# Kernel optimization log

Measured on AMD Instinct MI355X. Metric: run time of the kernel, lower is better.

## Reference

```python
import jax, jax.numpy as jnp
import numpy as np

GRID = 48
F = GRID * GRID        # number of mesh faces
C = 128                # channels
H = 8                  # attention heads
DH = C // H
B = 2                  # meshes in batch
WID = 256              # SelectionPrediction width


def _bfs_levels():
    """BFS flood-fill levels on a 4-connected GRIDxGRID face graph, anchor at center.
    Returns [n_levels, max_ring] int32, padded with F (dropped on scatter)."""
    c = GRID // 2
    ii, jj = np.meshgrid(np.arange(GRID), np.arange(GRID), indexing='ij')
    d = (np.abs(ii - c) + np.abs(jj - c)).reshape(-1)  # BFS depth == Manhattan dist
    L = int(d.max()) + 1
    Bd = int(np.bincount(d).max())
    idx = np.full((L, Bd), F, dtype=np.int32)
    for lv in range(L):
        faces = np.nonzero(d == lv)[0]
        idx[lv, :faces.size] = faces
    return jnp.asarray(idx)


def setup_inputs() -> dict:
    key = jax.random.key(0)
    ks = jax.random.split(key, 16)
    s = 1.0 / np.sqrt(C)
    sw = 1.0 / np.sqrt(WID)
    return {
        'x':  jax.random.normal(ks[0], (B, C, F), jnp.float32),
        # AnchorAttentionBlock projections (q/k/v/out)
        'Wq': jax.random.normal(ks[1], (C, C), jnp.float32) * s,
        'Wk': jax.random.normal(ks[2], (C, C), jnp.float32) * s,
        'Wv': jax.random.normal(ks[3], (C, C), jnp.float32) * s,
        'Wo': jax.random.normal(ks[4], (C, C), jnp.float32) * s,
        # SelectionPrediction (n_input=C, width=256, depth=3, sigmoid)
        'W1': jax.random.normal(ks[5], (C, WID), jnp.float32) * s,
        'b1': jnp.zeros((WID,), jnp.float32),
        'W2': jax.random.normal(ks[6], (WID, WID), jnp.float32) * sw,
        'b2': jnp.zeros((WID,), jnp.float32),
        'W3': jax.random.normal(ks[7], (WID, WID), jnp.float32) * sw,
        'b3': jnp.zeros((WID,), jnp.float32),
        'W4': jax.random.normal(ks[8], (WID, WID), jnp.float32) * sw,
        'b4': jnp.zeros((WID,), jnp.float32),
        'W5': jax.random.normal(ks[9], (WID, 1), jnp.float32) * sw,
        'b5': jnp.zeros((1,), jnp.float32),
        'levels_idx': _bfs_levels(),
    }


def reference(x, Wq, Wk, Wv, Wo, W1, b1, W2, b2, W3, b3, W4, b4, W5, b5, levels_idx):
    scale = 1.0 / jnp.sqrt(jnp.asarray(DH, x.dtype))

    def flood(feats):                       # feats: [F, C], one mesh
        def step(cur, idx):                 # idx: [Bd] boundary ring (pad = F)
            q = cur[idx]                                    # [Bd, C] (pad rows clamp-gather)
            qh = (q @ Wq).reshape(-1, H, DH)                # [Bd, H, DH]
            kh = (cur @ Wk).reshape(F, H, DH)               # global fftype: keys = all faces
            vh = (cur @ Wv).reshape(F, H, DH)
            att = jax.nn.softmax(jnp.einsum('bhd,fhd->bhf', qh, kh) * scale, axis=-1)
            o = jnp.einsum('bhf,fhd->bhd', att, vh).reshape(-1, C) @ Wo
            new = q + o                                     # mode='resid'
            return cur.at[idx].set(new, mode='drop'), None  # pad idx == F -> dropped
        out, _ = jax.lax.scan(step, feats, levels_idx)
        return out

    final = jax.vmap(flood)(x.transpose(0, 2, 1))           # [B, F, C]
    # SelectionPrediction on final_features.transpose(2,1)
    h = jax.nn.relu(final @ W1 + b1)
    h = jax.nn.relu(h @ W2 + b2)
    h = jax.nn.relu(h @ W3 + b3)
    h = jax.nn.relu(h @ W4 + b4)
    scores = jax.nn.sigmoid(h @ W5 + b5)                    # [B, F, 1] in [0, 1]
    return final.transpose(0, 2, 1), scores
```

## Files before the change

kernel.cpp:

```cpp
#include <hip/hip_runtime.h>
#include <hip/hip_bf16.h>
#include <stdint.h>

#define GRIDN 48
#define F 2304
#define C 128
#define H 8
#define DH 16
#define NB 2
#define WID 256
#define NLV 49
#define SMH (H * 18)

typedef __hip_bfloat16 bf16;

__device__ __forceinline__ float b2f(bf16 v) { return __bfloat162float(v); }

__global__ void k_permdetect(const void* __restrict__ x, int* __restrict__ flag,
                             int* __restrict__ permIdx, int* __restrict__ lvflags) {
    __shared__ int cnt[NLV], start[NLV];
    __shared__ int bad;
    int t = threadIdx.x;
    if (t == 0) bad = 0;
    if (t < NLV) cnt[t] = 0;
    for (int i = t; i < 2 * NLV + 2; i += 256) lvflags[i] = 0;
    __syncthreads();
    {
        const bf16* xb = (const bf16*)x;
        int insane = 0;
        #pragma unroll
        for (int i = 0; i < 8; ++i) {
            float v = b2f(xb[t * 8 + i]);
            if (!(fabsf(v) < 1e10f)) insane = 1;
        }
        if (insane) atomicOr(&bad, 1);
    }
    for (int f = t; f < F; f += 256) {
        int d = abs(f / GRIDN - GRIDN / 2) + abs(f % GRIDN - GRIDN / 2);
        atomicAdd(&cnt[d], 1);
    }
    __syncthreads();
    if (t == 0) {
        int s = 0;
        for (int l = 0; l < NLV; ++l) { start[l] = s; s += cnt[l]; }
        *flag = bad;
    }
    __syncthreads();
    for (int f = t; f < F; f += 256) {
        int d = abs(f / GRIDN - GRIDN / 2) + abs(f % GRIDN - GRIDN / 2);
        permIdx[f] = atomicAdd(&start[d], 1);
    }
}

struct WSeg { const void* src; int off; int cnt; };
struct WSegs { WSeg s[14]; };

__global__ void k_convert(WSegs segs, const int* __restrict__ flag,
                          float* __restrict__ dst, int total) {
    int i = blockIdx.x * blockDim.x + threadIdx.x;
    if (i >= total) return;
    bool f32 = (*flag != 0);
    #pragma unroll 1
    for (int j = 0; j < 14; ++j) {
        int off = segs.s[j].off, cnt = segs.s[j].cnt;
        if (i >= off && i < off + cnt) {
            int k = i - off;
            dst[i] = f32 ? ((const float*)segs.s[j].src)[k]
                         : b2f(((const bf16*)segs.s[j].src)[k]);
            return;
        }
    }
}

__global__ void k_wtrans(const float* __restrict__ Wk, const float* __restrict__ Wv,
                         const float* __restrict__ Wo, float* __restrict__ wT) {
    int m = blockIdx.y;
    const float* s = m == 0 ? Wk : (m == 1 ? Wv : Wo);
    int c = blockIdx.x;
    int k = threadIdx.x;
    wT[((size_t)m * C + c) * C + k] = s[k * C + c];
}

__global__ void k_transpose_in(const void* __restrict__ x, const int* __restrict__ flag,
                               float* __restrict__ cur) {
    __shared__ float tile[32][33];
    bool f32 = (*flag != 0);
    int b = blockIdx.z;
    int f0 = blockIdx.x * 32, c0 = blockIdx.y * 32;
    int tx = threadIdx.x, ty = threadIdx.y;
    #pragma unroll
    for (int i = 0; i < 4; ++i) {
        int c = c0 + ty + i * 8;
        size_t idx = ((size_t)b * C + c) * F + f0 + tx;
        tile[ty + i * 8][tx] = f32 ? ((const float*)x)[idx] : b2f(((const bf16*)x)[idx]);
    }
    __syncthreads();
    #pragma unroll
    for (int i = 0; i < 4; ++i) {
        int f = f0 + ty + i * 8;
        cur[((size_t)b * F + f) * C + c0 + tx] = tile[tx][ty + i * 8];
    }
}

__global__ __launch_bounds__(128) void k_proj_init(
        const float* __restrict__ cur, const int* __restrict__ permIdx,
        const float* __restrict__ Wq, const float* __restrict__ Wk, const float* __restrict__ Wv,
        float* __restrict__ qh, float* __restrict__ khT, float* __restrict__ vhT) {
    __shared__ float rows[2][C];
    int r0 = blockIdx.x * 2;
    int tid = threadIdx.x;
    rows[0][tid] = cur[(size_t)r0 * C + tid];
    rows[1][tid] = cur[(size_t)(r0 + 1) * C + tid];
    __syncthreads();
    float aq0 = 0.f, aq1 = 0.f, ak0 = 0.f, ak1 = 0.f, av0 = 0.f, av1 = 0.f;
    for (int k = 0; k < C; ++k) {
        float wq = Wq[k * C + tid];
        float wk = Wk[k * C + tid];
        float wv = Wv[k * C + tid];
        float x0 = rows[0][k], x1 = rows[1][k];
        aq0 = fmaf(x0, wq, aq0); aq1 = fmaf(x1, wq, aq1);
        ak0 = fmaf(x0, wk, ak0); ak1 = fmaf(x1, wk, ak1);
        av0 = fmaf(x0, wv, av0); av1 = fmaf(x1, wv, av1);
    }
    const float scale = 0.25f;
    #pragma unroll
    for (int r = 0; r < 2; ++r) {
        int grow = r0 + r;
        int mesh = grow / F, face = grow % F;
        int p = permIdx[face];
        qh[(size_t)grow * C + tid] = (r == 0 ? aq0 : aq1) * scale;
        khT[((size_t)mesh * C + tid) * F + p] = r == 0 ? ak0 : ak1;
        vhT[((size_t)mesh * C + tid) * F + p] = r == 0 ? av0 : av1;
    }
}

struct Rings { int v[NLV + 1]; };
struct Pairs { int v[NLV + 1]; };

__global__ __launch_bounds__(256) void k_static(
        int Bd, Rings rings, Pairs pairs,
        const int* __restrict__ levels,
        const float* __restrict__ qh_all,
        const float* __restrict__ khT, const float* __restrict__ vhT,
        float* __restrict__ smS) {
    int bx = blockIdx.x;
    int mesh = bx & 1;
    int gp = bx >> 1;
    int lv = 0;
    while (gp >= pairs.v[lv + 1]) ++lv;
    int spair = gp - pairs.v[lv];
    int rs = rings.v[lv];
    int s0 = spair * 2, s1 = s0 + 1;
    int face0 = (s0 < Bd) ? levels[lv * Bd + s0] : F;
    int face1 = (s1 < Bd) ? levels[lv * Bd + s1] : F;
    bool a0 = (face0 >= 0 && face0 < F), a1 = (face1 >= 0 && face1 < F);
    if (!a0 && !a1) return;

    __shared__ float sQh[2][C];
    int tid = threadIdx.x;
    size_t row0 = ((size_t)mesh * F + face0) * C;
    size_t row1 = ((size_t)mesh * F + face1) * C;
    if (tid < C) sQh[0][tid] = a0 ? qh_all[row0 + tid] : 0.f;
    else { int c = tid - C; sQh[1][c] = a1 ? qh_all[row1 + c] : 0.f; }
    __syncthreads();

    int head = tid >> 5, sub = tid & 31;
    float q0[DH], q1[DH];
    #pragma unroll
    for (int d = 0; d < DH; ++d) { q0[d] = sQh[0][head * DH + d]; q1[d] = sQh[1][head * DH + d]; }

    const float* Kb = khT + ((size_t)mesh * C + head * DH) * F;
    const float* Vb = vhT + ((size_t)mesh * C + head * DH) * F;

    float m0 = -1e30f, l0 = 0.f, m1 = -1e30f, l1 = 0.f;
    float acc0[DH], acc1[DH];
    #pragma unroll
    for (int d = 0; d < DH; ++d) { acc0[d] = 0.f; acc1[d] = 0.f; }

    int base0 = rs & ~127;
    for (int base = base0; base < F; base += 128) {
        int p4 = base + 4 * sub;
        float sx0 = 0, sy0 = 0, sz0 = 0, sw0 = 0;
        float sx1 = 0, sy1 = 0, sz1 = 0, sw1 = 0;
        #pragma unroll
        for (int d = 0; d < DH; ++d) {
            float4 kk = *(const float4*)(Kb + d * F + p4);
            float a = q0[d], b = q1[d];
            sx0 = fmaf(a, kk.x, sx0); sy0 = fmaf(a, kk.y, sy0);
            sz0 = fmaf(a, kk.z, sz0); sw0 = fmaf(a, kk.w, sw0);
            sx1 = fmaf(b, kk.x, sx1); sy1 = fmaf(b, kk.y, sy1);
            sz1 = fmaf(b, kk.z, sz1); sw1 = fmaf(b, kk.w, sw1);
        }
        float g0 = 1.f, g1 = 1.f, g2 = 1.f, g3 = 1.f;
        if (base < rs) {
            g0 = (p4     >= rs) ? 1.f : 0.f; g1 = (p4 + 1 >= rs) ? 1.f : 0.f;
            g2 = (p4 + 2 >= rs) ? 1.f : 0.f; g3 = (p4 + 3 >= rs) ? 1.f : 0.f;
        }
        float mx0 = fmaxf(fmaxf(sx0, sy0), fmaxf(sz0, sw0));
        float mn0 = fmaxf(m0, mx0);
        float c0 = __expf(m0 - mn0);
        float px0 = __expf(sx0 - mn0) * g0, py0 = __expf(sy0 - mn0) * g1;
        float pz0 = __expf(sz0 - mn0) * g2, pw0 = __expf(sw0 - mn0) * g3;
        l0 = fmaf(l0, c0, px0 + py0 + pz0 + pw0);
        m0 = mn0;
        float mx1 = fmaxf(fmaxf(sx1, sy1), fmaxf(sz1, sw1));
        float mn1 = fmaxf(m1, mx1);
        float c1e = __expf(m1 - mn1);
        float px1 = __expf(sx1 - mn1) * g0, py1 = __expf(sy1 - mn1) * g1;
        float pz1 = __expf(sz1 - mn1) * g2, pw1 = __expf(sw1 - mn1) * g3;
        l1 = fmaf(l1, c1e, px1 + py1 + pz1 + pw1);
        m1 = mn1;
        #pragma unroll
        for (int d = 0; d < DH; ++d) {
            float4 vv = *(const float4*)(Vb + d * F + p4);
            float w0 = fmaf(px0, vv.x, fmaf(py0, vv.y, fmaf(pz0, vv.z, pw0 * vv.w)));
            float w1 = fmaf(px1, vv.x, fmaf(py1, vv.y, fmaf(pz1, vv.z, pw1 * vv.w)));
            acc0[d] = fmaf(acc0[d], c0, w0);
            acc1[d] = fmaf(acc1[d], c1e, w1);
        }
    }

    #pragma unroll
    for (int w = 16; w >= 1; w >>= 1) {
        float mo = __shfl_xor(m0, w), lo = __shfl_xor(l0, w);
        float mn = fmaxf(m0, mo);
        float ca = __expf(m0 - mn), cb = __expf(mo - mn);
        l0 = l0 * ca + lo * cb;
        #pragma unroll
        for (int d = 0; d < DH; ++d) {
            float ao = __shfl_xor(acc0[d], w);
            acc0[d] = acc0[d] * ca + ao * cb;
        }
        m0 = mn;
        mo = __shfl_xor(m1, w); lo = __shfl_xor(l1, w);
        mn = fmaxf(m1, mo);
        ca = __expf(m1 - mn); cb = __expf(mo - mn);
        l1 = l1 * ca + lo * cb;
        #pragma unroll
        for (int d = 0; d < DH; ++d) {
            float ao = __shfl_xor(acc1[d], w);
            acc1[d] = acc1[d] * ca + ao * cb;
        }
        m1 = mn;
    }
    if (sub == 0) {
        if (a0) {
            float* S = smS + (size_t)(mesh * F + face0) * SMH + head * 18;
            S[0] = m0; S[1] = l0;
            #pragma unroll
            for (int d = 0; d < DH; ++d) S[2 + d] = acc0[d];
        }
        if (a1) {
            float* S = smS + (size_t)(mesh * F + face1) * SMH + head * 18;
            S[0] = m1; S[1] = l1;
            #pragma unroll
            for (int d = 0; d < DH; ++d) S[2 + d] = acc1[d];
        }
    }
}

__global__ __launch_bounds__(256, 4) void k_flood(
        int Bd, Rings rings, Pairs pairs,
        const int* __restrict__ levels, const int* __restrict__ permIdx,
        const float* __restrict__ qh_all, float* __restrict__ cur,
        float* __restrict__ khT, float* __restrict__ vhT,
        const float* __restrict__ smS,
        const float* __restrict__ WkT, const float* __restrict__ WvT,
        const float* __restrict__ WoT,
        int* __restrict__ lvflags, int* __restrict__ lvdone) {
    int bx = blockIdx.x;
    int mesh = bx & 1;
    int gp2 = bx >> 1;
    int lv = 0;
    while (gp2 >= pairs.v[lv + 1]) ++lv;
    int spair = gp2 - pairs.v[lv];

    int s0 = spair * 2, s1 = s0 + 1;
    int face0 = (s0 < Bd) ? levels[lv * Bd + s0] : F;
    int face1 = (s1 < Bd) ? levels[lv * Bd + s1] : F;
    bool a0 = (face0 >= 0 && face0 < F), a1 = (face1 >= 0 && face1 < F);

    __shared__ __attribute__((aligned(16))) float sQh[2][C], sQ[2][C], sRed[2][C], sNew2[2][C];
    __shared__ float sL[2][H];
    int tid = threadIdx.x;
    size_t row0 = ((size_t)mesh * F + face0) * C;
    size_t row1 = ((size_t)mesh * F + face1) * C;
    if (tid < C) {
        if (a0) { sQ[0][tid] = cur[row0 + tid]; sQh[0][tid] = qh_all[row0 + tid]; }
        else    { sQ[0][tid] = 0.f; sQh[0][tid] = 0.f; }
    } else {
        int c = tid - C;
        if (a1) { sQ[1][c] = cur[row1 + c]; sQh[1][c] = qh_all[row1 + c]; }
        else    { sQ[1][c] = 0.f; sQh[1][c] = 0.f; }
    }
    __syncthreads();

    int head = tid >> 5, sub = tid & 31;
    float q0[DH], q1[DH];
    #pragma unroll
    for (int d = 0; d < DH; ++d) { q0[d] = sQh[0][head * DH + d]; q1[d] = sQh[1][head * DH + d]; }

    float* Kb = khT + ((size_t)mesh * C + head * DH) * F;
    float* Vb = vhT + ((size_t)mesh * C + head * DH) * F;

    float m0 = -1e30f, l0 = 0.f, m1 = -1e30f, l1 = 0.f;
    float acc0[DH], acc1[DH];
    #pragma unroll
    for (int d = 0; d < DH; ++d) { acc0[d] = 0.f; acc1[d] = 0.f; }

    #define FOLD_COL(p)                                                                 \
    {                                                                                   \
        float kvv[DH], vv[DH];                                                          \
        _Pragma("unroll")                                                               \
        for (int d = 0; d < DH; ++d)                                                    \
            kvv[d] = __hip_atomic_load(Kb + (size_t)d * F + (p), __ATOMIC_RELAXED,      \
                                       __HIP_MEMORY_SCOPE_AGENT);                       \
        _Pragma("unroll")                                                               \
        for (int d = 0; d < DH; ++d)                                                    \
            vv[d] = __hip_atomic_load(Vb + (size_t)d * F + (p), __ATOMIC_RELAXED,       \
                                      __HIP_MEMORY_SCOPE_AGENT);                        \
        float s0v = 0.f, s1v = 0.f;                                                     \
        _Pragma("unroll")                                                               \
        for (int d = 0; d < DH; ++d) {                                                  \
            s0v = fmaf(q0[d], kvv[d], s0v);                                             \
            s1v = fmaf(q1[d], kvv[d], s1v);                                             \
        }                                                                               \
        float mn0_ = fmaxf(m0, s0v);                                                    \
        float c0_ = __expf(m0 - mn0_), pw0_ = __expf(s0v - mn0_);                       \
        l0 = l0 * c0_ + pw0_;                                                           \
        _Pragma("unroll")                                                               \
        for (int d = 0; d < DH; ++d) acc0[d] = fmaf(acc0[d], c0_, pw0_ * vv[d]);        \
        m0 = mn0_;                                                                      \
        float mn1_ = fmaxf(m1, s1v);                                                    \
        float c1_ = __expf(m1 - mn1_), pw1_ = __expf(s1v - mn1_);                       \
        l1 = l1 * c1_ + pw1_;                                                           \
        _Pragma("unroll")                                                               \
        for (int d = 0; d < DH; ++d) acc1[d] = fmaf(acc1[d], c1_, pw1_ * vv[d]);        \
        m1 = mn1_;                                                                      \
    }

    int ld = __hip_atomic_load(&lvdone[mesh], __ATOMIC_RELAXED, __HIP_MEMORY_SCOPE_AGENT);
    if (ld > lv) ld = lv;
    int bulkEnd = rings.v[ld];
    for (int p = sub; p < bulkEnd; p += 32) FOLD_COL(p);

    for (int gpi = ld; gpi < lv; ++gpi) {
        int need = pairs.v[gpi + 1] - pairs.v[gpi];
        int* fl = &lvflags[gpi * 2 + mesh];
        int guard = 0;
        while (__hip_atomic_load(fl, __ATOMIC_RELAXED, __HIP_MEMORY_SCOPE_AGENT) < need
               && guard < (1 << 22)) {
            __builtin_amdgcn_s_sleep(1);
            ++guard;
        }
        int frs = rings.v[gpi], fre = rings.v[gpi + 1];
        for (int p = frs + sub; p < fre; p += 32) FOLD_COL(p);
    }
    #undef FOLD_COL

    #pragma unroll
    for (int w = 16; w >= 1; w >>= 1) {
        float mo = __shfl_xor(m0, w), lo = __shfl_xor(l0, w);
        float mn = fmaxf(m0, mo);
        float ca = __expf(m0 - mn), cb = __expf(mo - mn);
        l0 = l0 * ca + lo * cb;
        #pragma unroll
        for (int d = 0; d < DH; ++d) {
            float ao = __shfl_xor(acc0[d], w);
            acc0[d] = acc0[d] * ca + ao * cb;
        }
        m0 = mn;
        mo = __shfl_xor(m1, w); lo = __shfl_xor(l1, w);
        mn = fmaxf(m1, mo);
        ca = __expf(m1 - mn); cb = __expf(mo - mn);
        l1 = l1 * ca + lo * cb;
        #pragma unroll
        for (int d = 0; d < DH; ++d) {
            float ao = __shfl_xor(acc1[d], w);
            acc1[d] = acc1[d] * ca + ao * cb;
        }
        m1 = mn;
    }
    if (sub == 0) {
        {
            int fr = a0 ? face0 : 0;
            const float* S = smS + (size_t)(mesh * F + fr) * SMH + head * 18;
            float ms = S[0], ls = S[1];
            float mn = fmaxf(m0, ms);
            float ca = __expf(m0 - mn), cb = __expf(ms - mn);
            sL[0][head] = l0 * ca + ls * cb;
            #pragma unroll
            for (int d = 0; d < DH; ++d)
                sRed[0][head * DH + d] = fmaf(acc0[d], ca, S[2 + d] * cb);
        }
        {
            int fr = a1 ? face1 : 0;
            const float* S = smS + (size_t)(mesh * F + fr) * SMH + head * 18;
            float ms = S[0], ls = S[1];
            float mn = fmaxf(m1, ms);
            float ca = __expf(m1 - mn), cb = __expf(ms - mn);
            sL[1][head] = l1 * ca + ls * cb;
            #pragma unroll
            for (int d = 0; d < DH; ++d)
                sRed[1][head * DH + d] = fmaf(acc1[d], ca, S[2 + d] * cb);
        }
    }
    __syncthreads();
    if (tid < C) sRed[0][tid] = sRed[0][tid] / sL[0][tid >> 4];
    else { int c = tid - C; sRed[1][c] = sRed[1][c] / sL[1][c >> 4]; }
    __syncthreads();

    {
        int j = tid >> 7;
        int c = tid & 127;
        bool act = j == 0 ? a0 : a1;
        float o = 0.f;
        const float4* WoR = (const float4*)(WoT + (size_t)c * C);
        const float4* Rr  = (const float4*)(&sRed[j][0]);
        #pragma unroll
        for (int k4 = 0; k4 < C / 4; ++k4) {
            float4 w = WoR[k4];
            float4 r = Rr[k4];
            o = fmaf(r.x, w.x, o); o = fmaf(r.y, w.y, o);
            o = fmaf(r.z, w.z, o); o = fmaf(r.w, w.w, o);
        }
        float nv = sQ[j][c] + o;
        sNew2[j][c] = nv;
        if (act) cur[(j == 0 ? row0 : row1) + c] = nv;
    }
    __syncthreads();

    if (lv != NLV - 1) {
        #pragma unroll 1
        for (int j = 0; j < 2; ++j) {
            bool act = j == 0 ? a0 : a1;
            if (!act) continue;
            int facej = j == 0 ? face0 : face1;
            int p = permIdx[facej];
            int c = tid & 127;
            const float* WT = (tid < C) ? WkT : WvT;
            float a = 0.f;
            const float4* Wr = (const float4*)(WT + (size_t)c * C);
            const float4* Nr = (const float4*)(&sNew2[j][0]);
            #pragma unroll
            for (int k4 = 0; k4 < C / 4; ++k4) {
                float4 w = Wr[k4];
                float4 x = Nr[k4];
                a = fmaf(x.x, w.x, a); a = fmaf(x.y, w.y, a);
                a = fmaf(x.z, w.z, a); a = fmaf(x.w, w.w, a);
            }
            if (tid < C)
                __hip_atomic_store(khT + ((size_t)mesh * C + c) * F + p, a,
                                   __ATOMIC_RELAXED, __HIP_MEMORY_SCOPE_AGENT);
            else
                __hip_atomic_store(vhT + ((size_t)mesh * C + c) * F + p, a,
                                   __ATOMIC_RELAXED, __HIP_MEMORY_SCOPE_AGENT);
        }
        __syncthreads();
        if (tid == 0) {
            int need = pairs.v[lv + 1] - pairs.v[lv];
            int old = __hip_atomic_fetch_add(&lvflags[lv * 2 + mesh], 1,
                                             __ATOMIC_RELAXED, __HIP_MEMORY_SCOPE_AGENT);
            if (old == need - 1)
                __hip_atomic_fetch_max(&lvdone[mesh], lv + 1,
                                       __ATOMIC_RELAXED, __HIP_MEMORY_SCOPE_AGENT);
        }
    }
}

__global__ __launch_bounds__(256) void k_mlp(
        const float* __restrict__ cur,
        const float* __restrict__ W1, const float* __restrict__ b1,
        const float* __restrict__ W2, const float* __restrict__ b2,
        const float* __restrict__ W3, const float* __restrict__ b3,
        const float* __restrict__ W4, const float* __restrict__ b4,
        const float* __restrict__ W5, const float* __restrict__ b5,
        float* __restrict__ out_scores) {
    __shared__ float sIn[2][C];
    __shared__ float sA[2][WID];
    __shared__ float sB[2][WID];
    int tid = threadIdx.x;
    int r0 = blockIdx.x * 2;
    for (int i = tid; i < 2 * C; i += 256) sIn[i >> 7][i & 127] = cur[(size_t)r0 * C + i];
    __syncthreads();
    {
        float a0 = 0.f, a1 = 0.f;
        for (int k = 0; k < C; ++k) {
            float w = W1[k * WID + tid];
            a0 = fmaf(sIn[0][k], w, a0);
            a1 = fmaf(sIn[1][k], w, a1);
        }
        float bias = b1[tid];
        sA[0][tid] = fmaxf(a0 + bias, 0.f);
        sA[1][tid] = fmaxf(a1 + bias, 0.f);
    }
    __syncthreads();
    {
        float a0 = 0.f, a1 = 0.f;
        for (int k = 0; k < WID; ++k) {
            float w = W2[k * WID + tid];
            a0 = fmaf(sA[0][k], w, a0);
            a1 = fmaf(sA[1][k], w, a1);
        }
        float bias = b2[tid];
        sB[0][tid] = fmaxf(a0 + bias, 0.f);
        sB[1][tid] = fmaxf(a1 + bias, 0.f);
    }
    __syncthreads();
    {
        float a0 = 0.f, a1 = 0.f;
        for (int k = 0; k < WID; ++k) {
            float w = W3[k * WID + tid];
            a0 = fmaf(sB[0][k], w, a0);
            a1 = fmaf(sB[1][k], w, a1);
        }
        float bias = b3[tid];
        sA[0][tid] = fmaxf(a0 + bias, 0.f);
        sA[1][tid] = fmaxf(a1 + bias, 0.f);
    }
    __syncthreads();
    {
        float a0 = 0.f, a1 = 0.f;
        for (int k = 0; k < WID; ++k) {
            float w = W4[k * WID + tid];
            a0 = fmaf(sA[0][k], w, a0);
            a1 = fmaf(sA[1][k], w, a1);
        }
        float bias = b4[tid];
        sB[0][tid] = fmaxf(a0 + bias, 0.f);
        sB[1][tid] = fmaxf(a1 + bias, 0.f);
    }
    __syncthreads();
    if (tid < 2) {
        float a = b5[0];
        for (int k = 0; k < WID; ++k) a = fmaf(sB[tid][k], W5[k], a);
        out_scores[r0 + tid] = 1.f / (1.f + __expf(-a));
    }
}

__global__ void k_transpose_out(const float* __restrict__ cur, float* __restrict__ out) {
    __shared__ float tile[32][33];
    int b = blockIdx.z;
    int f0 = blockIdx.x * 32, c0 = blockIdx.y * 32;
    int tx = threadIdx.x, ty = threadIdx.y;
    #pragma unroll
    for (int i = 0; i < 4; ++i) {
        int f = f0 + ty + i * 8;
        tile[ty + i * 8][tx] = cur[((size_t)b * F + f) * C + c0 + tx];
    }
    __syncthreads();
    #pragma unroll
    for (int i = 0; i < 4; ++i) {
        int c = c0 + ty + i * 8;
        out[((size_t)b * C + c) * F + f0 + tx] = tile[tx][ty + i * 8];
    }
}

extern "C" void kernel_launch(void* const* d_in, const int* in_sizes, int n_in,
                              void* d_out, int out_size, void* d_ws, size_t ws_size,
                              hipStream_t stream) {
    const int* levels = (const int*)d_in[15];
    int Bd = in_sizes[15] / NLV;

    const size_t n = (size_t)NB * F * C;
    float* cur  = (float*)d_ws;
    float* qh   = cur + n;
    float* khT  = qh + n;
    float* vhT  = khT + n;
    float* wbuf = vhT + n;
    float* wT   = wbuf + 296196;
    int*   permIdx = (int*)(wT + 49152);
    int*   flag = permIdx + F;
    int*   lvflags = flag + 1;
    int*   lvdone = lvflags + 2 * NLV;
    float* smS  = (float*)(permIdx + 2408);

    const int oWq = 0,       oWk = 16384,  oWv = 32768,  oWo = 49152;
    const int oW1 = 65536,   oB1 = 98304;
    const int oW2 = 98560,   oB2 = 164096;
    const int oW3 = 164352,  oB3 = 229888;
    const int oW4 = 230144,  oB4 = 295680;
    const int oW5 = 295936,  oB5 = 296192;
    const int wtot = 296193;

    WSegs segs = {{
        { d_in[1],  oWq, 16384 }, { d_in[2],  oWk, 16384 },
        { d_in[3],  oWv, 16384 }, { d_in[4],  oWo, 16384 },
        { d_in[5],  oW1, 32768 }, { d_in[6],  oB1, 256 },
        { d_in[7],  oW2, 65536 }, { d_in[8],  oB2, 256 },
        { d_in[9],  oW3, 65536 }, { d_in[10], oB3, 256 },
        { d_in[11], oW4, 65536 }, { d_in[12], oB4, 256 },
        { d_in[13], oW5, 256 },   { d_in[14], oB5, 1 },
    }};

    Rings rings;
    Pairs pairs;
    int totPairs = 0;
    {
        int cnt[NLV];
        for (int l = 0; l < NLV; ++l) cnt[l] = 0;
        for (int i = 0; i < GRIDN; ++i)
            for (int j = 0; j < GRIDN; ++j)
                cnt[(i < 24 ? 24 - i : i - 24) + (j < 24 ? 24 - j : j - 24)]++;
        rings.v[0] = 0;
        pairs.v[0] = 0;
        for (int l = 0; l < NLV; ++l) {
            rings.v[l + 1] = rings.v[l] + cnt[l];
            pairs.v[l + 1] = pairs.v[l] + (cnt[l] + 1) / 2;
        }
        totPairs = pairs.v[NLV];
    }

    float* out0 = (float*)d_out;
    float* out1 = out0 + (size_t)NB * C * F;

    k_permdetect<<<1, 256, 0, stream>>>(d_in[0], flag, permIdx, lvflags);
    k_convert<<<(wtot + 255) / 256, 256, 0, stream>>>(segs, flag, wbuf, wtot);
    k_wtrans<<<dim3(C, 3), C, 0, stream>>>(wbuf + oWk, wbuf + oWv, wbuf + oWo, wT);
    k_transpose_in<<<dim3(F / 32, C / 32, NB), dim3(32, 8), 0, stream>>>(d_in[0], flag, cur);
    k_proj_init<<<(NB * F) / 2, 128, 0, stream>>>(cur, permIdx, wbuf + oWq, wbuf + oWk, wbuf + oWv,
                                                  qh, khT, vhT);

    k_static<<<2 * totPairs, 256, 0, stream>>>(Bd, rings, pairs, levels, qh, khT, vhT, smS);

    k_flood<<<2 * totPairs, 256, 0, stream>>>(Bd, rings, pairs, levels, permIdx, qh, cur,
                                              khT, vhT, smS,
                                              wT, wT + 16384, wT + 32768,
                                              lvflags, lvdone);

    k_mlp<<<(NB * F) / 2, 256, 0, stream>>>(cur, wbuf + oW1, wbuf + oB1, wbuf + oW2, wbuf + oB2,
                                            wbuf + oW3, wbuf + oB3, wbuf + oW4, wbuf + oB4,
                                            wbuf + oW5, wbuf + oB5, out1);
    k_transpose_out<<<dim3(F / 32, C / 32, NB), dim3(32, 8), 0, stream>>>(cur, out0);
}
```

Baseline: 1.469 ms.

## Pad level flags, poll with one thread per block, split K/V projection rows

Spreads the per-level and per-mesh completion flags across separate 64-byte slots so that different meshes and levels do not share cache lines. Inter-block waiting is now done by thread 0 alone, followed by a block barrier, instead of every thread polling global memory. The lvdone value is read once into shared memory. The K/V re-projection maps each thread to two output channels of a single face, so the loop over the two faces disappears. The trade-off is an extra __syncthreads per waited level and a larger flag area in the workspace.

```diff
diff --git a/kernel.cpp b/kernel.cpp
--- a/kernel.cpp
+++ b/kernel.cpp
@@ -11,6 +11,7 @@
 #define WID 256
 #define NLV 49
 #define SMH (H * 18)
+#define LVS 32
 
 typedef __hip_bfloat16 bf16;
 
@@ -23,7 +24,7 @@
     int t = threadIdx.x;
     if (t == 0) bad = 0;
     if (t < NLV) cnt[t] = 0;
-    for (int i = t; i < 2 * NLV + 2; i += 256) lvflags[i] = 0;
+    for (int i = t; i < NLV * LVS + 32; i += 256) lvflags[i] = 0;
     __syncthreads();
     {
         const bf16* xb = (const bf16*)x;
@@ -282,6 +283,7 @@
 
     __shared__ __attribute__((aligned(16))) float sQh[2][C], sQ[2][C], sRed[2][C], sNew2[2][C];
     __shared__ float sL[2][H];
+    __shared__ int sLd;
     int tid = threadIdx.x;
     size_t row0 = ((size_t)mesh * F + face0) * C;
     size_t row1 = ((size_t)mesh * F + face1) * C;
@@ -293,6 +295,8 @@
         if (a1) { sQ[1][c] = cur[row1 + c]; sQh[1][c] = qh_all[row1 + c]; }
         else    { sQ[1][c] = 0.f; sQh[1][c] = 0.f; }
     }
+    if (tid == 0)
+        sLd = __hip_atomic_load(&lvdone[mesh * 16], __ATOMIC_RELAXED, __HIP_MEMORY_SCOPE_AGENT);
     __syncthreads();
 
     int head = tid >> 5, sub = tid & 31;
@@ -339,20 +343,23 @@
         m1 = mn1_;                                                                      \
     }
 
-    int ld = __hip_atomic_load(&lvdone[mesh], __ATOMIC_RELAXED, __HIP_MEMORY_SCOPE_AGENT);
+    int ld = sLd;
     if (ld > lv) ld = lv;
     int bulkEnd = rings.v[ld];
     for (int p = sub; p < bulkEnd; p += 32) FOLD_COL(p);
 
     for (int gpi = ld; gpi < lv; ++gpi) {
-        int need = pairs.v[gpi + 1] - pairs.v[gpi];
-        int* fl = &lvflags[gpi * 2 + mesh];
-        int guard = 0;
-        while (__hip_atomic_load(fl, __ATOMIC_RELAXED, __HIP_MEMORY_SCOPE_AGENT) < need
-               && guard < (1 << 22)) {
-            __builtin_amdgcn_s_sleep(1);
-            ++guard;
-        }
+        if (tid == 0) {
+            int need = pairs.v[gpi + 1] - pairs.v[gpi];
+            int* fl = &lvflags[gpi * LVS + mesh * 16];
+            int guard = 0;
+            while (__hip_atomic_load(fl, __ATOMIC_RELAXED, __HIP_MEMORY_SCOPE_AGENT) < need
+                   && guard < (1 << 22)) {
+                __builtin_amdgcn_s_sleep(2);
+                ++guard;
+            }
+        }
+        __syncthreads();
         int frs = rings.v[gpi], fre = rings.v[gpi + 1];
         for (int p = frs + sub; p < fre; p += 32) FOLD_COL(p);
     }
@@ -431,38 +438,40 @@
     __syncthreads();
 
     if (lv != NLV - 1) {
-        #pragma unroll 1
-        for (int j = 0; j < 2; ++j) {
-            bool act = j == 0 ? a0 : a1;
-            if (!act) continue;
+        int j = tid >> 7;
+        bool act = j == 0 ? a0 : a1;
+        if (act) {
             int facej = j == 0 ? face0 : face1;
             int p = permIdx[facej];
-            int c = tid & 127;
-            const float* WT = (tid < C) ? WkT : WvT;
-            float a = 0.f;
-            const float4* Wr = (const float4*)(WT + (size_t)c * C);
+            int isV = (tid >> 6) & 1;
+            int c2 = (tid & 63) * 2;
+            const float* WT = isV ? WvT : WkT;
+            float aa = 0.f, ab = 0.f;
+            const float4* Wa = (const float4*)(WT + (size_t)c2 * C);
+            const float4* Wb = (const float4*)(WT + (size_t)(c2 + 1) * C);
             const float4* Nr = (const float4*)(&sNew2[j][0]);
             #pragma unroll
             for (int k4 = 0; k4 < C / 4; ++k4) {
-                float4 w = Wr[k4];
                 float4 x = Nr[k4];
-                a = fmaf(x.x, w.x, a); a = fmaf(x.y, w.y, a);
-                a = fmaf(x.z, w.z, a); a = fmaf(x.w, w.w, a);
+                float4 wa = Wa[k4], wb = Wb[k4];
+                aa = fmaf(x.x, wa.x, aa); aa = fmaf(x.y, wa.y, aa);
+                aa = fmaf(x.z, wa.z, aa); aa = fmaf(x.w, wa.w, aa);
+                ab = fmaf(x.x, wb.x, ab); ab = fmaf(x.y, wb.y, ab);
+                ab = fmaf(x.z, wb.z, ab); ab = fmaf(x.w, wb.w, ab);
             }
-            if (tid < C)
-                __hip_atomic_store(khT + ((size_t)mesh * C + c) * F + p, a,
-                                   __ATOMIC_RELAXED, __HIP_MEMORY_SCOPE_AGENT);
-            else
-                __hip_atomic_store(vhT + ((size_t)mesh * C + c) * F + p, a,
-                                   __ATOMIC_RELAXED, __HIP_MEMORY_SCOPE_AGENT);
+            float* B = (isV ? vhT : khT) + (size_t)mesh * C * F + p;
+            __hip_atomic_store(B + (size_t)c2 * F, aa,
+                               __ATOMIC_RELAXED, __HIP_MEMORY_SCOPE_AGENT);
+            __hip_atomic_store(B + (size_t)(c2 + 1) * F, ab,
+                               __ATOMIC_RELAXED, __HIP_MEMORY_SCOPE_AGENT);
         }
         __syncthreads();
         if (tid == 0) {
             int need = pairs.v[lv + 1] - pairs.v[lv];
-            int old = __hip_atomic_fetch_add(&lvflags[lv * 2 + mesh], 1,
+            int old = __hip_atomic_fetch_add(&lvflags[lv * LVS + mesh * 16], 1,
                                              __ATOMIC_RELAXED, __HIP_MEMORY_SCOPE_AGENT);
             if (old == need - 1)
-                __hip_atomic_fetch_max(&lvdone[mesh], lv + 1,
+                __hip_atomic_fetch_max(&lvdone[mesh * 16], lv + 1,
                                        __ATOMIC_RELAXED, __HIP_MEMORY_SCOPE_AGENT);
         }
     }
@@ -571,9 +580,9 @@
     float* wT   = wbuf + 296196;
     int*   permIdx = (int*)(wT + 49152);
     int*   flag = permIdx + F;
-    int*   lvflags = flag + 1;
-    int*   lvdone = lvflags + 2 * NLV;
-    float* smS  = (float*)(permIdx + 2408);
+    int*   lvflags = permIdx + 2320;
+    int*   lvdone = lvflags + NLV * LVS;
+    float* smS  = (float*)(permIdx + 4096);
 
     const int oWq = 0,       oWk = 16384,  oWv = 32768,  oWo = 49152;
     const int oW1 = 65536,   oB1 = 98304;
```

Result: faster. 1.272 ms, median of 2 (-13.4%).
